# Optimization experiments

Measured on AMD Instinct MI355X. Metric: run time of the kernel, lower is better.

The kernel has to match this reference:

```python
import jax, jax.numpy as jnp
import numpy as np

B, C, H, W = 8, 512, 64, 64


def conv3x3(x, w, b):
    # x: [B,C,H,W], w: [O,I,3,3], b: [O]; stride 1, padding 1 (SAME)
    y = jax.lax.conv_general_dilated(
        x, w, window_strides=(1, 1), padding='SAME',
        dimension_numbers=('NCHW', 'OIHW', 'NCHW'))
    return y + b[None, :, None, None]


def setup_inputs() -> dict:
    key = jax.random.key(0)
    ks = jax.random.split(key, 8)
    wscale = 1.0 / np.sqrt(C * 9)  # keep attention logits in a sane range
    x = jax.random.normal(ks[0], (B, C, H, W), dtype=jnp.float32)
    wq = jax.random.normal(ks[1], (C, C, 3, 3), dtype=jnp.float32) * wscale
    bq = jax.random.normal(ks[2], (C,), dtype=jnp.float32) * 0.01
    wk = jax.random.normal(ks[3], (C, C, 3, 3), dtype=jnp.float32) * wscale
    bk = jax.random.normal(ks[4], (C,), dtype=jnp.float32) * 0.01
    wv = jax.random.normal(ks[5], (C, C, 3, 3), dtype=jnp.float32) * wscale
    bv = jax.random.normal(ks[6], (C,), dtype=jnp.float32) * 0.01
    gamma = jax.random.normal(ks[7], (1,), dtype=jnp.float32)
    return {'x': x, 'wq': wq, 'bq': bq, 'wk': wk, 'bk': bk,
            'wv': wv, 'bv': bv, 'gamma': gamma}


def reference(x, wq, bq, wk, bk, wv, bv, gamma):
    b, c, h, w = x.shape
    n = h * w
    q = conv3x3(x, wq, bq).reshape(b, c, n)   # [B,C,N]
    k = conv3x3(x, wk, bk).reshape(b, c, n)   # [B,C,N]
    v = conv3x3(x, wv, bv).reshape(b, c, n)   # [B,C,N]
    # channel-wise attention: [B,C,N] x [B,N,C] -> [B,C,C]
    attn = jnp.einsum('bcn,bdn->bcd', q, k)
    attn = jax.nn.softmax(attn, axis=-1)
    out = jnp.einsum('bcd,bdn->bcn', attn, v).reshape(b, c, h, w)
    return gamma * out + x
```

## Files before the change

kernel.cpp:

```cpp
#include <hip/hip_runtime.h>
#include <stdint.h>

typedef __attribute__((ext_vector_type(8))) short bf16x8;
typedef __attribute__((ext_vector_type(4))) float f32x4;
typedef __attribute__((ext_vector_type(2))) long i64x2;
typedef __attribute__((ext_vector_type(8))) unsigned short u16x8;
typedef __attribute__((ext_vector_type(4))) unsigned short u16x4;

#define DI static __device__ __forceinline__

constexpr int CB = 8;
constexpr int BCH = 4;
constexpr int CC = 512;
constexpr int CN = 4096;
constexpr int K1 = CC * 9;
constexpr int MR = 3 * CC;
constexpr int KSPL = 4;
constexpr size_t XSPLIT = (size_t)BCH * 66 * 66 * 512;

DI unsigned short f2bf(float f) {
  union { float f; uint32_t u; } v; v.f = f;
  uint32_t r = (v.u + 0x7FFFu + ((v.u >> 16) & 1u)) >> 16;
  return (unsigned short)r;
}
DI float bf2f(unsigned short h) {
  union { uint32_t u; float f; } v; v.u = ((uint32_t)h) << 16;
  return v.f;
}
DI unsigned char f2e4m3(float x) {
  union { float f; uint32_t u; } v; v.f = x;
  uint32_t sgn = (v.u >> 24) & 0x80u;
  float a = fabsf(x);
  if (a < 0.015625f) {
    int qi = (int)rintf(a * 512.f);
    return (unsigned char)(sgn | (uint32_t)qi);
  }
  int e = (int)((v.u >> 23) & 0xff) - 127;
  uint32_t m3 = (v.u >> 20) & 7u;
  uint32_t rest = v.u & 0xFFFFFu;
  if (rest > 0x80000u || (rest == 0x80000u && (m3 & 1u))) {
    if (++m3 == 8u) { m3 = 0; ++e; }
  }
  if (e > 8 || (e == 8 && m3 == 7u)) return (unsigned char)(sgn | 0x7Eu);
  return (unsigned char)(sgn | ((uint32_t)(e + 7) << 3) | m3);
}
DI int perm64(int k) { return (k & 7) + (((k >> 5) & 1) << 3) + (((k >> 3) & 3) << 4); }

DI void g2lds16(const void* g, void* l) {
  __builtin_amdgcn_global_load_lds((const __attribute__((address_space(1))) void*)g,
                                   (__attribute__((address_space(3))) void*)l, 16, 0, 0);
}
#define SBAR()  __builtin_amdgcn_s_barrier()
#define SCHED() __builtin_amdgcn_sched_barrier(0)

__global__ __launch_bounds__(256) void prep_xpad(const float* __restrict__ x,
                                                 unsigned short* __restrict__ Xhi,
                                                 unsigned char* __restrict__ X8) {
  int tid = threadIdx.x;
  int w = tid & 63;
  int ccl = tid >> 6;
  int blk = blockIdx.x;
  int h = blk & 63;
  int ccg = (blk >> 6) & 15;
  int b = blk >> 10;
  int c0 = (ccg * 4 + ccl) * 8;
  const float* xp = x + ((size_t)b * CC) * CN + h * 64 + w;
  u16x8 hi;
  unsigned long long lo8 = 0, hi8 = 0;
#pragma unroll
  for (int j = 0; j < 8; ++j) {
    float v = xp[(size_t)(c0 + j) * CN];
    unsigned short h16 = f2bf(v);
    float vhi = bf2f(h16);
    hi[j] = f2bf(vhi * 128.f);
    lo8 |= (unsigned long long)f2e4m3((v - vhi) * 256.f) << (8 * j);
    hi8 |= (unsigned long long)f2e4m3(vhi) << (8 * j);
  }
  size_t pix = (((size_t)b * 66 + (h + 1)) * 66 + (w + 1)) * 512;
  *(u16x8*)&Xhi[pix + c0] = hi;
  size_t p8 = pix + (size_t)(c0 & ~63) + perm64(c0 & 63);
  *(unsigned long long*)&X8[p8] = lo8;
  *(unsigned long long*)&X8[XSPLIT + p8] = hi8;
}

__global__ __launch_bounds__(256) void prep_abig(
    const float* __restrict__ wq, const float* __restrict__ wk,
    const float* __restrict__ wv, const float* __restrict__ bq,
    const float* __restrict__ bk, const float* __restrict__ bv,
    unsigned short* __restrict__ Ahi, unsigned char* __restrict__ A8,
    float* __restrict__ bias) {
  unsigned id = blockIdx.x * 256 + threadIdx.x;
  int m = id / K1;
  int r = id - m * K1;
  int t = r >> 9;
  int c = r & 511;
  int ky = t / 3;
  int kx = t - ky * 3;
  size_t ip = (size_t)m * 9216 + (size_t)(r & ~63) + perm64(r & 63);
  if (m < 1024) {
    const float* wp = (m < 512) ? wq : wk;
    int mm = (m < 512) ? m : m - 512;
    float wval = wp[(((size_t)mm * 512 + c) * 3 + ky) * 3 + kx];
    float whi = bf2f(f2bf(wval));
    Ahi[id] = f2bf(whi * 128.f);
    A8[ip] = f2e4m3(whi * 64.f);
    A8[ip + 4608] = f2e4m3((wval - whi) * 16384.f);
  } else {
    float wval = wv[(((size_t)(m - 1024) * 512 + c) * 3 + ky) * 3 + kx];
    Ahi[id] = f2bf(wval * 128.f);
    A8[ip] = 0;
    A8[ip + 4608] = 0;
  }
  if (id < 1536) {
    int mm = (int)id;
    bias[mm] = (mm < 512) ? bq[mm] : (mm < 1024) ? bk[mm - 512] : bv[mm - 1024];
  }
}

__global__ __launch_bounds__(512, 2) void conv_k(
    const unsigned short* __restrict__ Ahi,
    const unsigned char* __restrict__ A8,
    const unsigned short* __restrict__ Xhi,
    const unsigned char* __restrict__ X8,
    const float* __restrict__ bias,
    unsigned short* __restrict__ Qhi, unsigned short* __restrict__ Qlo,
    unsigned short* __restrict__ Khi, unsigned short* __restrict__ Klo,
    unsigned short* __restrict__ Vt)
{
  __shared__ __align__(16) unsigned char smem[4 * 32768];
  const int tid = threadIdx.x;
  const int lane = tid & 63;
  const int wid = tid >> 6;
  const int wr = wid >> 2;
  const int wc = wid & 3;

  int orig = blockIdx.x;
  int xcd, nbl, m0;
  if (orig < 256) {
    xcd = orig & 7; int j = orig >> 3;
    nbl = j >> 2;
    m0 = (j & 3) * 256;
  } else {
    int o = orig - 256;
    xcd = o & 7; int j = o >> 3;
    nbl = j >> 2;
    m0 = 1024 + (j & 3) * 128;
  }
  const int nb = xcd * 8 + nbl;
  const int n0 = nb * 256;
  const int bidx = n0 >> 12;
  const int nl0 = n0 & (CN - 1);
  const int h0 = nl0 >> 6;

  const int srow = tid >> 2;
  const int scu = tid & 3;
  const int scuS = scu ^ ((srow >> 1) & 3);
  const size_t pixOfs = (((size_t)(bidx * 66 + h0 + (srow >> 6))) * 66 + (srow & 63)) * 512;
  const unsigned short* gAh0 = Ahi + (size_t)(m0 + srow) * K1 + scuS * 8;
  const unsigned short* gAh1 = gAh0 + (size_t)128 * K1;
  const unsigned short* gBh0 = Xhi + pixOfs + scuS * 8;
  const unsigned short* gBh1 = gBh0 + (size_t)2 * 66 * 512;
  const unsigned char* gA80 = A8 + (size_t)(m0 + srow) * 9216 + scuS * 16;
  const unsigned char* gA81 = gA80 + (size_t)128 * 9216;
  const unsigned char* gB80 = X8 + pixOfs + scuS * 16;
  const unsigned char* gB81 = gB80 + (size_t)2 * 66 * 512;
  const int wofs = wid * 1024;

  int c0S = 0, kxS = 0, tapS = 0;
  size_t tapOfs = 0;
  auto stage1 = [&](int slot) {
    int aOfs = tapS * 512 + c0S;
    size_t bOfs = tapOfs + (size_t)c0S;
    unsigned char* lA = smem + slot * 32768 + wofs;
    unsigned char* lB = smem + slot * 32768 + 16384 + wofs;
    g2lds16(gAh0 + aOfs, lA);
    g2lds16(gAh1 + aOfs, lA + 8192);
    g2lds16(gBh0 + bOfs, lB);
    g2lds16(gBh1 + bOfs, lB + 8192);
    c0S += 32;
    if (c0S == 512) {
      c0S = 0; ++tapS;
      if (kxS == 2) { kxS = 0; tapOfs += (size_t)64 * 512; }
      else { ++kxS; tapOfs += 512; }
    }
  };
  auto stage1v = [&](int slot) {
    int aOfs = tapS * 512 + c0S;
    size_t bOfs = tapOfs + (size_t)c0S;
    unsigned char* lA = smem + slot * 32768 + wofs;
    unsigned char* lB = smem + slot * 32768 + 16384 + wofs;
    g2lds16(gAh0 + aOfs, lA);
    g2lds16(gBh0 + bOfs, lB);
    g2lds16(gBh1 + bOfs, lB + 8192);
    c0S += 32;
    if (c0S == 512) {
      c0S = 0; ++tapS;
      if (kxS == 2) { kxS = 0; tapOfs += (size_t)64 * 512; }
      else { ++kxS; tapOfs += 512; }
    }
  };
  int c8 = 0, kx8 = 0, tap8 = 0, s8 = 0;
  size_t tapOfs8 = 0;
  auto stage2 = [&](int slot) {
    int aOfs = s8 * 4608 + tap8 * 512 + c8;
    size_t bOfs = (size_t)s8 * XSPLIT + tapOfs8 + (size_t)c8;
    unsigned char* lA = smem + slot * 32768 + wofs;
    unsigned char* lB = smem + slot * 32768 + 16384 + wofs;
    g2lds16(gA80 + aOfs, lA);
    g2lds16(gA81 + aOfs, lA + 8192);
    g2lds16(gB80 + bOfs, lB);
    g2lds16(gB81 + bOfs, lB + 8192);
    c8 += 64;
    if (c8 == 512) {
      c8 = 0; ++tap8;
      if (tap8 == 9) { tap8 = 0; kx8 = 0; tapOfs8 = 0; ++s8; }
      else if (kx8 == 2) { kx8 = 0; tapOfs8 += (size_t)64 * 512; }
      else { ++kx8; tapOfs8 += 512; }
    }
  };

  f32x4 acc[8][4];
  const f32x4 fz = {0.f, 0.f, 0.f, 0.f};
#pragma unroll
  for (int i = 0; i < 8; ++i)
#pragma unroll
    for (int j = 0; j < 4; ++j) acc[i][j] = fz;

  const int kq = (lane >> 4) * 16;
  int slotC, slotS, t2;

  if (m0 < 1024) {
    const int rA = wr * 128 + (lane & 15);
    const int rB = wc * 64 + (lane & 15);
    const int kqA = kq ^ (((rA >> 1) & 3) << 4);
    const int kqB = kq ^ (((rB >> 1) & 3) << 4);

    stage1(0);
    stage1(1);
    asm volatile("s_waitcnt vmcnt(4)" ::: "memory");
    SCHED(); SBAR(); SCHED();
    {
      bf16x8 afA[4], bfA[4], afB[4], bfB[4], af1[4];
#pragma unroll
      for (int mf = 0; mf < 4; ++mf)
        afA[mf] = *(const bf16x8*)(smem + (rA + mf * 16) * 64 + kqA);
#pragma unroll
      for (int nf = 0; nf < 4; ++nf)
        bfA[nf] = *(const bf16x8*)(smem + 16384 + (rB + nf * 16) * 64 + kqB);
      slotC = 0; slotS = 2; t2 = 2;

#define CONV_BF(CURA, CURB, NXTA, NXTB)                                       \
  {                                                                           \
    if (t2 < 144) {                                                           \
      stage1(slotS); slotS = (slotS + 1) & 3;                                 \
      asm volatile("s_waitcnt vmcnt(4)" ::: "memory");                        \
    } else {                                                                  \
      asm volatile("s_waitcnt vmcnt(0)" ::: "memory");                        \
    }                                                                         \
    SCHED(); SBAR(); SCHED();                                                 \
    const unsigned char* lA = smem + slotC * 32768;                           \
    const int slotN = (slotC + 1) & 3;                                        \
    const unsigned char* lAn = smem + slotN * 32768;                          \
    _Pragma("unroll")                                                         \
    for (int mf = 0; mf < 4; ++mf)                                            \
      af1[mf] = *(const bf16x8*)(lA + (rA + 64 + mf * 16) * 64 + kqA);        \
    __builtin_amdgcn_s_setprio(1);                                            \
    _Pragma("unroll")                                                         \
    for (int mf = 0; mf < 4; ++mf) {                                          \
      _Pragma("unroll")                                                       \
      for (int nf = 0; nf < 4; ++nf)                                          \
        acc[mf][nf] = __builtin_amdgcn_mfma_f32_16x16x32_bf16(                \
            CURA[mf], CURB[nf], acc[mf][nf], 0, 0, 0);                        \
    }                                                                         \
    __builtin_amdgcn_s_setprio(0);                                            \
    _Pragma("unroll")                                                         \
    for (int mf = 0; mf < 4; ++mf)                                            \
      NXTA[mf] = *(const bf16x8*)(lAn + (rA + mf * 16) * 64 + kqA);           \
    _Pragma("unroll")                                                         \
    for (int nf = 0; nf < 4; ++nf)                                            \
      NXTB[nf] = *(const bf16x8*)(lAn + 16384 + (rB + nf * 16) * 64 + kqB);   \
    __builtin_amdgcn_s_setprio(1);                                            \
    _Pragma("unroll")                                                         \
    for (int mf = 0; mf < 4; ++mf) {                                          \
      _Pragma("unroll")                                                       \
      for (int nf = 0; nf < 4; ++nf)                                          \
        acc[mf + 4][nf] = __builtin_amdgcn_mfma_f32_16x16x32_bf16(            \
            af1[mf], CURB[nf], acc[mf + 4][nf], 0, 0, 0);                     \
    }                                                                         \
    __builtin_amdgcn_s_setprio(0);                                            \
    slotC = slotN;                                                            \
    ++t2;                                                                     \
  }

      for (int t = 0; t < 144; t += 2) {
        CONV_BF(afA, bfA, afB, bfB)
        CONV_BF(afB, bfB, afA, bfA)
      }
#undef CONV_BF
    }

    {
      stage2(0);
      stage2(1);
      asm volatile("s_waitcnt vmcnt(4)" ::: "memory");
      SCHED(); SBAR(); SCHED();
      i64x2 a8A[4], b8A[4], a8B[4], b8B[4], a18[4];
#pragma unroll
      for (int mf = 0; mf < 4; ++mf)
        a8A[mf] = *(const i64x2*)(smem + (rA + mf * 16) * 64 + kqA);
#pragma unroll
      for (int nf = 0; nf < 4; ++nf)
        b8A[nf] = *(const i64x2*)(smem + 16384 + (rB + nf * 16) * 64 + kqB);
      slotC = 0; slotS = 2; t2 = 2;

#define CONV_F8(CURA, CURB, NXTA, NXTB)                                       \
  {                                                                           \
    if (t2 < 144) {                                                           \
      stage2(slotS); slotS = (slotS + 1) & 3;                                 \
      asm volatile("s_waitcnt vmcnt(4)" ::: "memory");                        \
    } else {                                                                  \
      asm volatile("s_waitcnt vmcnt(0)" ::: "memory");                        \
    }                                                                         \
    SCHED(); SBAR(); SCHED();                                                 \
    const unsigned char* lA = smem + slotC * 32768;                           \
    const int slotN = (slotC + 1) & 3;                                        \
    const unsigned char* lAn = smem + slotN * 32768;                          \
    _Pragma("unroll")                                                         \
    for (int mf = 0; mf < 4; ++mf)                                            \
      a18[mf] = *(const i64x2*)(lA + (rA + 64 + mf * 16) * 64 + kqA);         \
    __builtin_amdgcn_s_setprio(1);                                            \
    _Pragma("unroll")                                                         \
    for (int mf = 0; mf < 4; ++mf) {                                          \
      _Pragma("unroll")                                                       \
      for (int nf = 0; nf < 4; ++nf) {                                        \
        acc[mf][nf] = __builtin_amdgcn_mfma_f32_16x16x32_fp8_fp8(             \
            CURA[mf][0], CURB[nf][0], acc[mf][nf], 0, 0, 0);                  \
        acc[mf][nf] = __builtin_amdgcn_mfma_f32_16x16x32_fp8_fp8(             \
            CURA[mf][1], CURB[nf][1], acc[mf][nf], 0, 0, 0);                  \
      }                                                                       \
    }                                                                         \
    __builtin_amdgcn_s_setprio(0);                                            \
    _Pragma("unroll")                                                         \
    for (int mf = 0; mf < 4; ++mf)                                            \
      NXTA[mf] = *(const i64x2*)(lAn + (rA + mf * 16) * 64 + kqA);            \
    _Pragma("unroll")                                                         \
    for (int nf = 0; nf < 4; ++nf)                                            \
      NXTB[nf] = *(const i64x2*)(lAn + 16384 + (rB + nf * 16) * 64 + kqB);    \
    __builtin_amdgcn_s_setprio(1);                                            \
    _Pragma("unroll")                                                         \
    for (int mf = 0; mf < 4; ++mf) {                                          \
      _Pragma("unroll")                                                       \
      for (int nf = 0; nf < 4; ++nf) {                                        \
        acc[mf + 4][nf] = __builtin_amdgcn_mfma_f32_16x16x32_fp8_fp8(         \
            a18[mf][0], CURB[nf][0], acc[mf + 4][nf], 0, 0, 0);               \
        acc[mf + 4][nf] = __builtin_amdgcn_mfma_f32_16x16x32_fp8_fp8(         \
            a18[mf][1], CURB[nf][1], acc[mf + 4][nf], 0, 0, 0);               \
      }                                                                       \
    }                                                                         \
    __builtin_amdgcn_s_setprio(0);                                            \
    slotC = slotN;                                                            \
    ++t2;                                                                     \
  }

      for (int t = 0; t < 144; t += 2) {
        CONV_F8(a8A, b8A, a8B, b8B)
        CONV_F8(a8B, b8B, a8A, b8A)
      }
#undef CONV_F8
    }
  } else {
    const int rAv = wr * 64 + (lane & 15);
    const int rB = wc * 64 + (lane & 15);
    const int kqA = kq ^ (((rAv >> 1) & 3) << 4);
    const int kqB = kq ^ (((rB >> 1) & 3) << 4);

    stage1v(0);
    stage1v(1);
    asm volatile("s_waitcnt vmcnt(3)" ::: "memory");
    SCHED(); SBAR(); SCHED();
    bf16x8 afA[4], bfA[4], afB[4], bfB[4];
#pragma unroll
    for (int mf = 0; mf < 4; ++mf)
      afA[mf] = *(const bf16x8*)(smem + (rAv + mf * 16) * 64 + kqA);
#pragma unroll
    for (int nf = 0; nf < 4; ++nf)
      bfA[nf] = *(const bf16x8*)(smem + 16384 + (rB + nf * 16) * 64 + kqB);
    slotC = 0; slotS = 2; t2 = 2;

#define CONV_LV(CURA, CURB, NXTA, NXTB)                                       \
  {                                                                           \
    if (t2 < 144) {                                                           \
      stage1v(slotS); slotS = (slotS + 1) & 3;                                \
      asm volatile("s_waitcnt vmcnt(3)" ::: "memory");                        \
    } else {                                                                  \
      asm volatile("s_waitcnt vmcnt(0)" ::: "memory");                        \
    }                                                                         \
    SCHED(); SBAR(); SCHED();                                                 \
    const int slotN = (slotC + 1) & 3;                                        \
    const unsigned char* lAn = smem + slotN * 32768;                          \
    _Pragma("unroll")                                                         \
    for (int mf = 0; mf < 4; ++mf)                                            \
      NXTA[mf] = *(const bf16x8*)(lAn + (rAv + mf * 16) * 64 + kqA);          \
    _Pragma("unroll")                                                         \
    for (int nf = 0; nf < 4; ++nf)                                            \
      NXTB[nf] = *(const bf16x8*)(lAn + 16384 + (rB + nf * 16) * 64 + kqB);   \
    __builtin_amdgcn_s_setprio(1);                                            \
    _Pragma("unroll")                                                         \
    for (int mf = 0; mf < 4; ++mf) {                                          \
      _Pragma("unroll")                                                       \
      for (int nf = 0; nf < 4; ++nf)                                          \
        acc[mf][nf] = __builtin_amdgcn_mfma_f32_16x16x32_bf16(                \
            CURA[mf], CURB[nf], acc[mf][nf], 0, 0, 0);                        \
    }                                                                         \
    __builtin_amdgcn_s_setprio(0);                                            \
    slotC = slotN;                                                            \
    ++t2;                                                                     \
  }

    for (int t = 0; t < 144; t += 2) {
      CONV_LV(afA, bfA, afB, bfB)
      CONV_LV(afB, bfB, afA, bfA)
    }
#undef CONV_LV
  }

  constexpr float SC = 1.f / 16384.f;
  if (m0 < 1024) {
#pragma unroll
    for (int mf = 0; mf < 8; ++mf) {
#pragma unroll
      for (int nf = 0; nf < 4; ++nf) {
        f32x4 a = acc[mf][nf];
        int mrow = m0 + wr * 128 + mf * 16 + ((lane >> 4) << 2);
        int ncol = nl0 + wc * 64 + nf * 16 + (lane & 15);
        if (m0 < 512) {
#pragma unroll
          for (int j = 0; j < 4; ++j) {
            float v = a[j] * SC + bias[mrow + j];
            unsigned short h16 = f2bf(v);
            size_t o = ((size_t)bidx * CC + (mrow + j)) * CN + ncol;
            Qhi[o] = h16;
            Qlo[o] = f2bf(v - bf2f(h16));
          }
        } else {
#pragma unroll
          for (int j = 0; j < 4; ++j) {
            float v = a[j] * SC + bias[mrow + j];
            unsigned short h16 = f2bf(v);
            size_t o = ((size_t)bidx * CC + (mrow + j - 512)) * CN + ncol;
            Khi[o] = h16;
            Klo[o] = f2bf(v - bf2f(h16));
          }
        }
      }
    }
  } else {
#pragma unroll
    for (int mf = 0; mf < 4; ++mf) {
#pragma unroll
      for (int nf = 0; nf < 4; ++nf) {
        f32x4 a = acc[mf][nf];
        int mrow = m0 + wr * 64 + mf * 16 + ((lane >> 4) << 2);
        int ncol = nl0 + wc * 64 + nf * 16 + (lane & 15);
        u16x4 vs;
#pragma unroll
        for (int j = 0; j < 4; ++j) vs[j] = f2bf(a[j] * SC + bias[mrow + j]);
        *(u16x4*)&Vt[((size_t)bidx * CN + ncol) * CC + (mrow - 1024)] = vs;
      }
    }
  }
}

DI int sofs(int row, int kb) { return row * 128 + (kb ^ ((row & 7) << 4)); }

template<int MODE>
__global__ __launch_bounds__(256) void gemm_k(
    const unsigned short* __restrict__ Qhi, const unsigned short* __restrict__ Qlo,
    const unsigned short* __restrict__ Khi, const unsigned short* __restrict__ Klo,
    const unsigned short* __restrict__ Vt,
    float* __restrict__ attn,
    const unsigned short* __restrict__ P,
    const float* __restrict__ xin,
    const float* __restrict__ gamma,
    float* __restrict__ out)
{
  __shared__ __align__(16) unsigned char sA[16384];
  __shared__ __align__(16) unsigned char sB[16384];
  const int tid = threadIdx.x;
  const int lane = tid & 63;
  const int wav = tid >> 6;
  const int wr = wav >> 1, wc = wav & 1;

  int m0, n0, bidx, Kbeg = 0, Kend, ks = 0;
  if constexpr (MODE == 1) {
    int tile = blockIdx.x & 15;
    ks = blockIdx.x >> 4;
    m0 = (tile & 3) * 128;
    n0 = (tile >> 2) * 128;
    bidx = blockIdx.z;
    Kbeg = ks * (3 * CN / KSPL);
    Kend = Kbeg + (3 * CN / KSPL);
  } else {
    m0 = (blockIdx.x & 3) * 128;
    n0 = (blockIdx.x >> 2) * 128;
    bidx = blockIdx.z;
    Kend = CC;
  }

  auto stage = [&](int k0) {
#pragma unroll
    for (int q = 0; q < 4; ++q) {
      int ci = q * 256 + tid;
      int row = ci >> 3;
      int ke = ((ci & 7) ^ (row & 7)) * 8;
      const unsigned short* ap;
      const unsigned short* bp;
      if constexpr (MODE == 1) {
        int ph = k0 >> 12;
        int kin = k0 & (CN - 1);
        const unsigned short* Aq = (ph == 2) ? Qlo : Qhi;
        const unsigned short* Bk = (ph == 1) ? Klo : Khi;
        ap = Aq + ((size_t)bidx * CC + (m0 + row)) * CN + (kin + ke);
        bp = Bk + ((size_t)bidx * CC + (n0 + row)) * CN + (kin + ke);
      } else {
        ap = P + ((size_t)bidx * CC + (m0 + row)) * CC + (k0 + ke);
        bp = Vt + ((size_t)bidx * CN + (n0 + row)) * CC + (k0 + ke);
      }
      int wbase = (q * 256 + wav * 64) * 16;
      g2lds16(ap, sA + wbase);
      g2lds16(bp, sB + wbase);
    }
  };

  f32x4 acc[4][4];
  const f32x4 fz = {0.f, 0.f, 0.f, 0.f};
#pragma unroll
  for (int i = 0; i < 4; ++i)
#pragma unroll
    for (int j = 0; j < 4; ++j) acc[i][j] = fz;

  for (int k0 = Kbeg; k0 < Kend; k0 += 64) {
    stage(k0);
    __syncthreads();
#pragma unroll
    for (int kkp = 0; kkp < 2; ++kkp) {
      bf16x8 af[4], bfv[4];
#pragma unroll
      for (int mf = 0; mf < 4; ++mf)
        af[mf] = *(const bf16x8*)&sA[sofs(wr * 64 + mf * 16 + (lane & 15),
                                          kkp * 64 + (lane >> 4) * 16)];
#pragma unroll
      for (int nf = 0; nf < 4; ++nf)
        bfv[nf] = *(const bf16x8*)&sB[sofs(wc * 64 + nf * 16 + (lane & 15),
                                           kkp * 64 + (lane >> 4) * 16)];
#pragma unroll
      for (int mf = 0; mf < 4; ++mf)
#pragma unroll
        for (int nf = 0; nf < 4; ++nf)
          acc[mf][nf] = __builtin_amdgcn_mfma_f32_16x16x32_bf16(
              af[mf], bfv[nf], acc[mf][nf], 0, 0, 0);
    }
    __syncthreads();
  }

  float g = 0.f;
  if constexpr (MODE == 2) g = gamma[0];
#pragma unroll
  for (int mf = 0; mf < 4; ++mf) {
#pragma unroll
    for (int nf = 0; nf < 4; ++nf) {
      f32x4 a = acc[mf][nf];
      int mrow = m0 + wr * 64 + mf * 16 + ((lane >> 4) << 2);
      int ncol = n0 + wc * 64 + nf * 16 + (lane & 15);
      if constexpr (MODE == 1) {
        size_t pbase = (size_t)ks * ((size_t)BCH * CC * CC);
#pragma unroll
        for (int j = 0; j < 4; ++j)
          attn[pbase + ((size_t)bidx * CC + (mrow + j)) * CC + ncol] = a[j];
      } else {
#pragma unroll
        for (int j = 0; j < 4; ++j) {
          size_t o = ((size_t)bidx * CC + (mrow + j)) * CN + ncol;
          out[o] = g * a[j] + xin[o];
        }
      }
    }
  }
}

__global__ __launch_bounds__(256) void softmax_k(const float* __restrict__ attn,
                                                 unsigned short* __restrict__ P) {
  int row = blockIdx.x * 4 + (threadIdx.x >> 6);
  int lane = threadIdx.x & 63;
  constexpr size_t PS = (size_t)BCH * CC * CC;
  const float* rp = attn + (size_t)row * 512 + lane * 8;
  f32x4 a = {0.f, 0.f, 0.f, 0.f};
  f32x4 b = {0.f, 0.f, 0.f, 0.f};
#pragma unroll
  for (int ksp = 0; ksp < KSPL; ++ksp) {
    a += *(const f32x4*)(rp + (size_t)ksp * PS);
    b += *(const f32x4*)(rp + (size_t)ksp * PS + 4);
  }
  float mx = fmaxf(fmaxf(fmaxf(a[0], a[1]), fmaxf(a[2], a[3])),
                   fmaxf(fmaxf(b[0], b[1]), fmaxf(b[2], b[3])));
#pragma unroll
  for (int s = 32; s > 0; s >>= 1) mx = fmaxf(mx, __shfl_xor(mx, s, 64));
  float e[8];
  float sum = 0.f;
#pragma unroll
  for (int j = 0; j < 4; ++j) { e[j] = __expf(a[j] - mx); sum += e[j]; }
#pragma unroll
  for (int j = 0; j < 4; ++j) { e[4 + j] = __expf(b[j] - mx); sum += e[4 + j]; }
#pragma unroll
  for (int s = 32; s > 0; s >>= 1) sum += __shfl_xor(sum, s, 64);
  float inv = 1.0f / sum;
  u16x8 o;
#pragma unroll
  for (int j = 0; j < 8; ++j) o[j] = f2bf(e[j] * inv);
  *(u16x8*)&P[(size_t)row * 512 + lane * 8] = o;
}

__global__ __launch_bounds__(256) void fill_sentinel(float* __restrict__ out, int n) {
  int i = blockIdx.x * 256 + threadIdx.x;
  if (i < n) out[i] = 1.0e4f;
}

extern "C" void kernel_launch(void* const* d_in, const int* in_sizes, int n_in,
                              void* d_out, int out_size, void* d_ws, size_t ws_size,
                              hipStream_t stream) {
  (void)in_sizes; (void)n_in;
  const float* x  = (const float*)d_in[0];
  const float* wq = (const float*)d_in[1];
  const float* bq = (const float*)d_in[2];
  const float* wk = (const float*)d_in[3];
  const float* bk = (const float*)d_in[4];
  const float* wv = (const float*)d_in[5];
  const float* bv = (const float*)d_in[6];
  const float* gm = (const float*)d_in[7];
  float* out = (float*)d_out;

  uint8_t* wsp = (uint8_t*)d_ws;
  auto take = [&](size_t bytes) {
    uint8_t* p = wsp;
    wsp += (bytes + 255) & ~(size_t)255;
    return p;
  };
  unsigned short* Xhi = (unsigned short*)take(XSPLIT * 2);
  unsigned char*  X8  = (unsigned char*)take(2 * XSPLIT);
  unsigned short* Ahi = (unsigned short*)take((size_t)MR * K1 * 2);
  unsigned char*  A8  = (unsigned char*)take((size_t)MR * 2 * K1);
  float* bias         = (float*)take((size_t)MR * 4);
  unsigned short* Khi = (unsigned short*)take((size_t)BCH * CC * CN * 2);
  unsigned short* Klo = (unsigned short*)take((size_t)BCH * CC * CN * 2);
  unsigned short* Vt  = (unsigned short*)take((size_t)BCH * CN * CC * 2);
  float* attn         = (float*)Xhi;
  unsigned short* P   = (unsigned short*)((uint8_t*)Xhi +
                          (size_t)KSPL * BCH * CC * CC * 4 + 256);

  size_t needed = (size_t)(wsp - (uint8_t*)d_ws);
  if (ws_size < needed) {
    fill_sentinel<<<(out_size + 255) / 256, 256, 0, stream>>>(out, out_size);
    return;
  }

  for (int ch = 0; ch < CB / BCH; ++ch) {
    const float* xch = x + (size_t)ch * BCH * CC * CN;
    float* outch = out + (size_t)ch * BCH * CC * CN;
    unsigned short* Qhi = (unsigned short*)outch;
    unsigned short* Qlo = Qhi + (size_t)BCH * CC * CN;

    hipMemsetAsync(Xhi, 0, XSPLIT * 2 + 2 * XSPLIT, stream);
    prep_xpad<<<BCH * 16 * 64, 256, 0, stream>>>(xch, Xhi, X8);
    if (ch == 0)
      prep_abig<<<(MR * K1) / 256, 256, 0, stream>>>(wq, wk, wv, bq, bk, bv,
                                                     Ahi, A8, bias);
    conv_k<<<dim3(512), 512, 0, stream>>>(Ahi, A8, Xhi, X8, bias,
                                          Qhi, Qlo, Khi, Klo, Vt);
    gemm_k<1><<<dim3(16 * KSPL, 1, BCH), 256, 0, stream>>>(Qhi, Qlo, Khi, Klo, Vt,
                                                           attn, P, xch, gm, outch);
    softmax_k<<<BCH * 128, 256, 0, stream>>>(attn, P);
    gemm_k<2><<<dim3(128, 1, BCH), 256, 0, stream>>>(Qhi, Qlo, Khi, Klo, Vt,
                                                     attn, P, xch, gm, outch);
  }
}
```

Measured before the change: 1.054 ms.

## Use MFMA scale 16x16x128 fp8 instructions for the fp8 correction conv pass

Replaces the fp8 correction pass of the conv GEMM, which used 16x16x32 fp8 MFMAs, with the gfx950 scaled 16x16x128 f8f6f4 MFMA (unit scales). Each loop iteration now consumes two LDS stages, double-buffered in 64KB halves, and the stage-ahead schedule changes to match. The channel permutation (perm64) in the fp8 pack kernels is removed so LDS reads take contiguous 16-byte chunks under the existing XOR swizzle. This is meant to cut MFMA instruction count and LDS-read and barrier overhead, at the risk of fragment-layout mismatches and less overlap between loads and compute.

```diff
diff --git a/kernel.cpp b/kernel.cpp
--- a/kernel.cpp
+++ b/kernel.cpp
@@ -3,7 +3,8 @@
 
 typedef __attribute__((ext_vector_type(8))) short bf16x8;
 typedef __attribute__((ext_vector_type(4))) float f32x4;
-typedef __attribute__((ext_vector_type(2))) long i64x2;
+typedef __attribute__((ext_vector_type(4))) int i32x4;
+typedef __attribute__((ext_vector_type(8))) int i32x8;
 typedef __attribute__((ext_vector_type(8))) unsigned short u16x8;
 typedef __attribute__((ext_vector_type(4))) unsigned short u16x4;
 
@@ -44,7 +45,6 @@
   if (e > 8 || (e == 8 && m3 == 7u)) return (unsigned char)(sgn | 0x7Eu);
   return (unsigned char)(sgn | ((uint32_t)(e + 7) << 3) | m3);
 }
-DI int perm64(int k) { return (k & 7) + (((k >> 5) & 1) << 3) + (((k >> 3) & 3) << 4); }
 
 DI void g2lds16(const void* g, void* l) {
   __builtin_amdgcn_global_load_lds((const __attribute__((address_space(1))) void*)g,
@@ -78,9 +78,8 @@
   }
   size_t pix = (((size_t)b * 66 + (h + 1)) * 66 + (w + 1)) * 512;
   *(u16x8*)&Xhi[pix + c0] = hi;
-  size_t p8 = pix + (size_t)(c0 & ~63) + perm64(c0 & 63);
-  *(unsigned long long*)&X8[p8] = lo8;
-  *(unsigned long long*)&X8[XSPLIT + p8] = hi8;
+  *(unsigned long long*)&X8[pix + c0] = lo8;
+  *(unsigned long long*)&X8[XSPLIT + pix + c0] = hi8;
 }
 
 __global__ __launch_bounds__(256) void prep_abig(
@@ -96,7 +95,7 @@
   int c = r & 511;
   int ky = t / 3;
   int kx = t - ky * 3;
-  size_t ip = (size_t)m * 9216 + (size_t)(r & ~63) + perm64(r & 63);
+  size_t ip = (size_t)m * 9216 + r;
   if (m < 1024) {
     const float* wp = (m < 512) ? wq : wk;
     int mm = (m < 512) ? m : m - 512;
@@ -299,74 +298,60 @@
 #undef CONV_BF
     }
 
+    stage2(0); stage2(1);
+    SCHED(); SBAR(); SCHED();
+    stage2(2); stage2(3);
     {
-      stage2(0);
-      stage2(1);
-      asm volatile("s_waitcnt vmcnt(4)" ::: "memory");
-      SCHED(); SBAR(); SCHED();
-      i64x2 a8A[4], b8A[4], a8B[4], b8B[4], a18[4];
-#pragma unroll
-      for (int mf = 0; mf < 4; ++mf)
-        a8A[mf] = *(const i64x2*)(smem + (rA + mf * 16) * 64 + kqA);
-#pragma unroll
-      for (int nf = 0; nf < 4; ++nf)
-        b8A[nf] = *(const i64x2*)(smem + 16384 + (rB + nf * 16) * 64 + kqB);
-      slotC = 0; slotS = 2; t2 = 2;
-
-#define CONV_F8(CURA, CURB, NXTA, NXTB)                                       \
-  {                                                                           \
-    if (t2 < 144) {                                                           \
-      stage2(slotS); slotS = (slotS + 1) & 3;                                 \
-      asm volatile("s_waitcnt vmcnt(4)" ::: "memory");                        \
-    } else {                                                                  \
-      asm volatile("s_waitcnt vmcnt(0)" ::: "memory");                        \
-    }                                                                         \
-    SCHED(); SBAR(); SCHED();                                                 \
-    const unsigned char* lA = smem + slotC * 32768;                           \
-    const int slotN = (slotC + 1) & 3;                                        \
-    const unsigned char* lAn = smem + slotN * 32768;                          \
-    _Pragma("unroll")                                                         \
-    for (int mf = 0; mf < 4; ++mf)                                            \
-      a18[mf] = *(const i64x2*)(lA + (rA + 64 + mf * 16) * 64 + kqA);         \
-    __builtin_amdgcn_s_setprio(1);                                            \
-    _Pragma("unroll")                                                         \
-    for (int mf = 0; mf < 4; ++mf) {                                          \
-      _Pragma("unroll")                                                       \
-      for (int nf = 0; nf < 4; ++nf) {                                        \
-        acc[mf][nf] = __builtin_amdgcn_mfma_f32_16x16x32_fp8_fp8(             \
-            CURA[mf][0], CURB[nf][0], acc[mf][nf], 0, 0, 0);                  \
-        acc[mf][nf] = __builtin_amdgcn_mfma_f32_16x16x32_fp8_fp8(             \
-            CURA[mf][1], CURB[nf][1], acc[mf][nf], 0, 0, 0);                  \
-      }                                                                       \
-    }                                                                         \
-    __builtin_amdgcn_s_setprio(0);                                            \
-    _Pragma("unroll")                                                         \
-    for (int mf = 0; mf < 4; ++mf)                                            \
-      NXTA[mf] = *(const i64x2*)(lAn + (rA + mf * 16) * 64 + kqA);            \
-    _Pragma("unroll")                                                         \
-    for (int nf = 0; nf < 4; ++nf)                                            \
-      NXTB[nf] = *(const i64x2*)(lAn + 16384 + (rB + nf * 16) * 64 + kqB);    \
-    __builtin_amdgcn_s_setprio(1);                                            \
-    _Pragma("unroll")                                                         \
-    for (int mf = 0; mf < 4; ++mf) {                                          \
-      _Pragma("unroll")                                                       \
-      for (int nf = 0; nf < 4; ++nf) {                                        \
-        acc[mf + 4][nf] = __builtin_amdgcn_mfma_f32_16x16x32_fp8_fp8(         \
-            a18[mf][0], CURB[nf][0], acc[mf + 4][nf], 0, 0, 0);               \
-        acc[mf + 4][nf] = __builtin_amdgcn_mfma_f32_16x16x32_fp8_fp8(         \
-            a18[mf][1], CURB[nf][1], acc[mf + 4][nf], 0, 0, 0);               \
-      }                                                                       \
-    }                                                                         \
-    __builtin_amdgcn_s_setprio(0);                                            \
-    slotC = slotN;                                                            \
-    ++t2;                                                                     \
-  }
-
-      for (int t = 0; t < 144; t += 2) {
-        CONV_F8(a8A, b8A, a8B, b8B)
-        CONV_F8(a8B, b8B, a8A, b8A)
+      const int gq = lane >> 4;
+      const int slotByte = (gq >> 1) << 15;
+      const int cb2 = (gq & 1) * 2;
+      const int ff2 = ((lane & 15) >> 1) & 3;
+      const int bo0 = ((cb2 ^ ff2) << 4);
+      const int bo1 = (((cb2 + 1) ^ ff2) << 4);
+      const int aRow = wr * 128 + (lane & 15);
+      const int bRow = wc * 64 + (lane & 15);
+      i32x8 aF[4], bF[4];
+      for (int p = 0; p < 72; ++p) {
+        SCHED(); SBAR(); SCHED();
+        if (p < 71) { asm volatile("s_waitcnt vmcnt(8)" ::: "memory"); }
+        else        { asm volatile("s_waitcnt vmcnt(0)" ::: "memory"); }
+        SCHED();
+        const unsigned char* pbA = smem + ((p & 1) << 16) + slotByte + aRow * 64;
+        const unsigned char* pbB = smem + ((p & 1) << 16) + slotByte + 16384 + bRow * 64;
+#pragma unroll
+        for (int t = 0; t < 4; ++t) {
+          *(i32x4*)&bF[t] = *(const i32x4*)(pbB + t * 1024 + bo0);
+          *((i32x4*)&bF[t] + 1) = *(const i32x4*)(pbB + t * 1024 + bo1);
+        }
+#pragma unroll
+        for (int s = 0; s < 4; ++s) {
+          *(i32x4*)&aF[s] = *(const i32x4*)(pbA + s * 1024 + bo0);
+          *((i32x4*)&aF[s] + 1) = *(const i32x4*)(pbA + s * 1024 + bo1);
+        }
+        __builtin_amdgcn_s_setprio(1);
+#pragma unroll
+        for (int s = 0; s < 4; ++s)
+#pragma unroll
+          for (int t = 0; t < 4; ++t)
+            acc[s][t] = __builtin_amdgcn_mfma_scale_f32_16x16x128_f8f6f4(
+                aF[s], bF[t], acc[s][t], 0, 0, 0, 127, 0, 127);
+        __builtin_amdgcn_s_setprio(0);
+#pragma unroll
+        for (int s = 0; s < 4; ++s) {
+          *(i32x4*)&aF[s] = *(const i32x4*)(pbA + (4 + s) * 1024 + bo0);
+          *((i32x4*)&aF[s] + 1) = *(const i32x4*)(pbA + (4 + s) * 1024 + bo1);
+        }
+        __builtin_amdgcn_s_setprio(1);
+#pragma unroll
+        for (int s = 0; s < 4; ++s)
+#pragma unroll
+          for (int t = 0; t < 4; ++t)
+            acc[s + 4][t] = __builtin_amdgcn_mfma_scale_f32_16x16x128_f8f6f4(
+                aF[s], bF[t], acc[s + 4][t], 0, 0, 0, 127, 0, 127);
+        __builtin_amdgcn_s_setprio(0);
+        SCHED(); SBAR(); SCHED();
+        if (p + 2 < 72) { stage2(2 * (p & 1)); stage2(2 * (p & 1) + 1); }
       }
-#undef CONV_F8
     }
   } else {
     const int rAv = wr * 64 + (lane & 15);
```

New measurement: 1.007 ms. -4.4%, faster.
